# Kernel optimization log

Measured on AMD Instinct MI355X. Metric: run time of the kernel, lower is better.

Reference implementation:

```python
import jax, jax.numpy as jnp
import numpy as np

N_BINS = 20


def setup_inputs() -> dict:
    key = jax.random.key(0)
    k1, k2 = jax.random.split(key)
    softmaxes = jax.random.uniform(k1, (1000000, 100), dtype=jnp.float32)
    labels = jax.random.randint(k2, (1000000,), 0, 100, dtype=jnp.int64)
    return {"softmaxes": softmaxes, "labels": labels}


def reference(softmaxes, labels):
    num = softmaxes.shape[0]
    window = num // N_BINS  # equal-frequency bin size

    confidences = jnp.max(softmaxes, axis=1)
    predictions = jnp.argmax(softmaxes, axis=1)
    accuracies = (predictions == labels).astype(softmaxes.dtype)

    order = jnp.argsort(confidences)  # ascending, like torch.sort
    conf_sorted = confidences[order]
    acc_sorted = accuracies[order]

    # only full windows are flushed in the original loop
    n_used = N_BINS * window
    conf_bins = conf_sorted[:n_used].reshape(N_BINS, window)
    acc_bins = acc_sorted[:n_used].reshape(N_BINS, window)

    avg_conf = conf_bins.mean(axis=1)  # [N_BINS]
    avg_acc = acc_bins.mean(axis=1)    # [N_BINS] == ys list

    ece = jnp.sum(jnp.abs(avg_conf - avg_acc)) * (window / num)
    return ece.reshape(1), avg_acc
```

## Files before the change

### kernel.cpp

```cpp
#include <hip/hip_runtime.h>
#include <hip/hip_bf16.h>
#include <math.h>
#include <stdint.h>

#define NROWS 1000000
#define NCOLS 100
#define NBINS 20
#define NB    19
#define W     50000u
#define NH    2049

#define HIST_DW 0u
#define BINS_DW 2052u
#define ZERO_DW 2132u
#define CONF_DW 2136u

#define GLOAD_LDS16(g, l) __builtin_amdgcn_global_load_lds(                    \
    (const __attribute__((address_space(1))) void*)(g),                        \
    (__attribute__((address_space(3))) void*)(l), 16, 0, 0)

__device__ __forceinline__ unsigned int bucket_of(unsigned int bits) {
    if (bits < 0x3F000000u) return 0u;
    unsigned int t = (bits >> 12) - 258048u + 1u;
    return t > 2048u ? 2048u : t;
}

__global__ __launch_bounds__(256) void k1_rowmax(const float* __restrict__ x,
                                                 const int* __restrict__ labels,
                                                 float* __restrict__ conf,
                                                 unsigned int* __restrict__ zero_region) {
    __shared__ float4 ldsx4[1600];
    __shared__ unsigned long long ldsk[64];
    const float* ldsx = (const float*)ldsx4;
    int tid = threadIdx.x;
    int gtid = blockIdx.x * 256 + tid;
    if (gtid < (int)ZERO_DW) zero_region[gtid] = 0u;

    const int NTILES = NROWS / 64;
    const float4* xb = reinterpret_cast<const float4*>(x);
    for (int tile = blockIdx.x; tile < NTILES; tile += gridDim.x) {
        const float4* src = xb + (size_t)tile * 1600;
        int lab = 0;
        if (tid < 64) lab = labels[tile * 64 + tid];
        int wbase = tid & 192;
        #pragma unroll
        for (int i = 0; i < 6; i++) {
            int v = i * 256 + tid;
            GLOAD_LDS16(src + v, ldsx4 + i * 256 + wbase);
        }
        if (tid < 64) GLOAD_LDS16(src + 1536 + tid, ldsx4 + 1536);
        if (tid < 64) ldsk[tid] = 0ull;
        __syncthreads();
        int r = tid >> 2, q = tid & 3;
        const float* rowp = ldsx + r * 100 + q * 25;
        float best = rowp[0]; int bi = 0;
        #pragma unroll
        for (int k = 1; k < 25; k++) {
            float vv = rowp[k];
            if (vv > best) { best = vv; bi = k; }
        }
        unsigned long long key =
            ((unsigned long long)__float_as_uint(best) << 32)
            | (unsigned int)(NCOLS - (q * 25 + bi));
        atomicMax(&ldsk[r], key);
        __syncthreads();
        if (tid < 64) {
            unsigned long long kk = ldsk[tid];
            unsigned int bits = (unsigned int)(kk >> 32);
            int idx = NCOLS - (int)(kk & 0xFFFFFFFFu);
            if (idx == lab) bits |= 0x80000000u;
            conf[tile * 64 + tid] = __uint_as_float(bits);
        }
        __syncthreads();
    }
}

__global__ __launch_bounds__(512) void k2_hist(const float* __restrict__ conf,
                                               unsigned int* __restrict__ hist) {
    __shared__ unsigned int lh[NH];
    for (int i = threadIdx.x; i < NH; i += 512) lh[i] = 0u;
    __syncthreads();
    const uint4* c4 = reinterpret_cast<const uint4*>(conf);
    int stride = gridDim.x * 512;
    for (int i = blockIdx.x * 512 + threadIdx.x; i < NROWS / 4; i += stride) {
        uint4 v = c4[i];
        atomicAdd(&lh[bucket_of(v.x & 0x7FFFFFFFu)], 1u);
        atomicAdd(&lh[bucket_of(v.y & 0x7FFFFFFFu)], 1u);
        atomicAdd(&lh[bucket_of(v.z & 0x7FFFFFFFu)], 1u);
        atomicAdd(&lh[bucket_of(v.w & 0x7FFFFFFFu)], 1u);
    }
    __syncthreads();
    for (int i = threadIdx.x; i < NH; i += 512) {
        unsigned int c = lh[i];
        if (c) atomicAdd(&hist[i], c);
    }
}

__global__ __launch_bounds__(256) void k3_accum(const float* __restrict__ conf,
                                                const unsigned int* __restrict__ hist,
                                                double* __restrict__ bins) {
    __shared__ unsigned int ptab[NH];
    __shared__ unsigned int s[256];
    __shared__ unsigned int bndS[NB];
    __shared__ float sFr[NB];
    __shared__ float sc[4][NBINS], sa[4][NBINS];
    int tid = threadIdx.x;

    unsigned int loc[9];
    unsigned int tot = 0;
    int base = tid * 9;
    #pragma unroll
    for (int k = 0; k < 9; k++) {
        int idx = base + k;
        unsigned int v = (idx < NH) ? hist[idx] : 0u;
        loc[k] = tot; tot += v;
    }
    s[tid] = tot; __syncthreads();
    for (int off = 1; off < 256; off <<= 1) {
        unsigned int v = (tid >= off) ? s[tid - off] : 0u;
        __syncthreads();
        s[tid] += v;
        __syncthreads();
    }
    unsigned int excl = s[tid] - tot;
    #pragma unroll
    for (int k = 0; k < 9; k++) {
        int idx = base + k;
        if (idx < NH) ptab[idx] = excl + loc[k];
    }
    for (int i = tid; i < 4 * NBINS; i += 256) { (&sc[0][0])[i] = 0.f; (&sa[0][0])[i] = 0.f; }
    __syncthreads();

    if (tid < NB) {
        unsigned int r = (unsigned int)(tid + 1) * W;
        int lo = 0, hi = NH - 1;
        while (lo < hi) {
            int mid = (lo + hi + 1) >> 1;
            if (ptab[mid] <= r) lo = mid; else hi = mid - 1;
        }
        unsigned int p = ptab[lo];
        if (p < r) {
            unsigned int cnt = ((lo + 1 < NH) ? ptab[lo + 1] : (unsigned int)NROWS) - p;
            bndS[tid] = (unsigned int)lo;
            sFr[tid]  = (float)(r - p) / (float)cnt;
        } else {
            bndS[tid] = 0xFFFFFFFFu;
        }
    }
    __syncthreads();
    if (tid < NB && bndS[tid] != 0xFFFFFFFFu)
        ptab[bndS[tid]] |= (unsigned int)(tid + 1) << 24;
    __syncthreads();

    int wid = tid >> 6;
    const uint4* c4 = reinterpret_cast<const uint4*>(conf);
    int stride = gridDim.x * 256;
    for (int i = blockIdx.x * 256 + tid; i < NROWS / 4; i += stride) {
        uint4 q = c4[i];
        unsigned int bs[4] = { q.x, q.y, q.z, q.w };
        #pragma unroll
        for (int j = 0; j < 4; j++) {
            unsigned int raw = bs[j];
            float a = (float)(raw >> 31);
            unsigned int bits = raw & 0x7FFFFFFFu;
            float c = __uint_as_float(bits);
            unsigned int e = ptab[bucket_of(bits)];
            unsigned int t = e >> 24;
            if (t == 0u) {
                unsigned int bin = (e & 0xFFFFFFu) / W;
                atomicAdd(&sc[wid][bin], c); atomicAdd(&sa[wid][bin], a);
            } else {
                float fr = sFr[t - 1];
                atomicAdd(&sc[wid][t - 1], c * fr);
                atomicAdd(&sc[wid][t],     c * (1.f - fr));
                atomicAdd(&sa[wid][t - 1], a * fr);
                atomicAdd(&sa[wid][t],     a * (1.f - fr));
            }
        }
    }
    __syncthreads();
    if (tid < NBINS) {
        float tc = sc[0][tid] + sc[1][tid] + sc[2][tid] + sc[3][tid];
        float ta = sa[0][tid] + sa[1][tid] + sa[2][tid] + sa[3][tid];
        atomicAdd(&bins[tid],         (double)tc);
        atomicAdd(&bins[NBINS + tid], (double)ta);
    }
}

__global__ __launch_bounds__(64) void k4_final(const double* __restrict__ bins,
                                               float* __restrict__ out) {
    if (threadIdx.x == 0) {
        double ece = 0.0;
        for (int b = 0; b < NBINS; b++) {
            double avc = bins[b] / (double)W;
            double ava = bins[NBINS + b] / (double)W;
            ece += fabs(avc - ava);
            out[1 + b] = (float)ava;
        }
        out[0] = (float)(ece * ((double)W / (double)NROWS));
    }
}

extern "C" void kernel_launch(void* const* d_in, const int* in_sizes, int n_in,
                              void* d_out, int out_size, void* d_ws, size_t ws_size,
                              hipStream_t stream) {
    const float* x      = (const float*)d_in[0];
    const int*   labels = (const int*)d_in[1];
    float*       out    = (float*)d_out;
    unsigned int* wd    = (unsigned int*)d_ws;

    unsigned int* hist = wd + HIST_DW;
    double*       bins = (double*)(wd + BINS_DW);
    float*        conf = (float*)(wd + CONF_DW);

    k1_rowmax<<<2048, 256, 0, stream>>>(x, labels, conf, wd);
    k2_hist  <<<128, 512, 0, stream>>>(conf, hist);
    k3_accum <<<512, 256, 0, stream>>>(conf, hist, bins);
    k4_final <<<1, 64, 0, stream>>>(bins, out);
}
```

Before: 115.7 us.

## Double-buffer row tiles in rowmax kernel and use shuffle argmax reduction

The row-max kernel now double-buffers LDS tiles, issuing async global-to-LDS loads for the next tile before computing on the current one, with explicit vmcnt waits and raw barriers. The 64-bit LDS atomicMax reduction is replaced by intra-quad shuffle reductions that keep the lowest index on ties. Each thread that owns a row loads its label directly. The aim is to hide global load latency in this memory-bound pass and cut barriers and LDS atomics. The cost is double the LDS per block, which may lower occupancy, and fragile manual waitcnt handling.

```diff
diff --git a/kernel.cpp b/kernel.cpp
--- a/kernel.cpp
+++ b/kernel.cpp
@@ -29,50 +29,71 @@
                                                  const int* __restrict__ labels,
                                                  float* __restrict__ conf,
                                                  unsigned int* __restrict__ zero_region) {
-    __shared__ float4 ldsx4[1600];
-    __shared__ unsigned long long ldsk[64];
-    const float* ldsx = (const float*)ldsx4;
+    __shared__ float4 ldsx4[3200];
     int tid = threadIdx.x;
     int gtid = blockIdx.x * 256 + tid;
     if (gtid < (int)ZERO_DW) zero_region[gtid] = 0u;
 
     const int NTILES = NROWS / 64;
     const float4* xb = reinterpret_cast<const float4*>(x);
-    for (int tile = blockIdx.x; tile < NTILES; tile += gridDim.x) {
-        const float4* src = xb + (size_t)tile * 1600;
-        int lab = 0;
-        if (tid < 64) lab = labels[tile * 64 + tid];
-        int wbase = tid & 192;
-        #pragma unroll
-        for (int i = 0; i < 6; i++) {
-            int v = i * 256 + tid;
-            GLOAD_LDS16(src + v, ldsx4 + i * 256 + wbase);
-        }
-        if (tid < 64) GLOAD_LDS16(src + 1536 + tid, ldsx4 + 1536);
-        if (tid < 64) ldsk[tid] = 0ull;
-        __syncthreads();
-        int r = tid >> 2, q = tid & 3;
-        const float* rowp = ldsx + r * 100 + q * 25;
+    int lane = tid & 63;
+    int w    = tid >> 6;
+    int lab_next = 0, lab_cur = 0;
+
+    float4* bufA = ldsx4;
+    float4* bufB = ldsx4 + 1600;
+
+#define K1_ISSUE(t, buf)                                                       \
+    do {                                                                       \
+        const float4* src_ = xb + (size_t)(t) * 1600;                          \
+        _Pragma("unroll")                                                      \
+        for (int i_ = 0; i_ < 6; i_++)                                         \
+            GLOAD_LDS16(src_ + i_ * 256 + tid, (buf) + i_ * 256 + (tid & 192));\
+        if (lane < 16)                                                         \
+            GLOAD_LDS16(src_ + 1536 + 16 * w + lane, (buf) + 1536 + 16 * w);   \
+        if ((tid & 3) == 0) lab_next = labels[(t) * 64 + (tid >> 2)];          \
+    } while (0)
+
+    int tile = blockIdx.x;
+    if (tile < NTILES) K1_ISSUE(tile, bufA);
+
+    while (tile < NTILES) {
+        lab_cur = lab_next;
+        int nxt = tile + gridDim.x;
+        if (nxt < NTILES) {
+            K1_ISSUE(nxt, bufB);
+            asm volatile("s_waitcnt vmcnt(8)" ::: "memory");
+        } else {
+            asm volatile("s_waitcnt vmcnt(0)" ::: "memory");
+        }
+        __builtin_amdgcn_sched_barrier(0);
+        __builtin_amdgcn_s_barrier();
+
+        const float* rowp = (const float*)bufA + (tid >> 2) * 100 + (tid & 3) * 25;
         float best = rowp[0]; int bi = 0;
         #pragma unroll
         for (int k = 1; k < 25; k++) {
             float vv = rowp[k];
             if (vv > best) { best = vv; bi = k; }
         }
-        unsigned long long key =
-            ((unsigned long long)__float_as_uint(best) << 32)
-            | (unsigned int)(NCOLS - (q * 25 + bi));
-        atomicMax(&ldsk[r], key);
-        __syncthreads();
-        if (tid < 64) {
-            unsigned long long kk = ldsk[tid];
-            unsigned int bits = (unsigned int)(kk >> 32);
-            int idx = NCOLS - (int)(kk & 0xFFFFFFFFu);
-            if (idx == lab) bits |= 0x80000000u;
-            conf[tile * 64 + tid] = __uint_as_float(bits);
-        }
-        __syncthreads();
-    }
+        bi += (tid & 3) * 25;
+        #pragma unroll
+        for (int mask = 1; mask <= 2; mask <<= 1) {
+            float ov = __shfl_xor(best, mask);
+            int   oi = __shfl_xor(bi,   mask);
+            if (ov > best || (ov == best && oi < bi)) { best = ov; bi = oi; }
+        }
+        if ((tid & 3) == 0) {
+            unsigned int bits = __float_as_uint(best);
+            if (bi == lab_cur) bits |= 0x80000000u;
+            conf[tile * 64 + (tid >> 2)] = __uint_as_float(bits);
+        }
+        __builtin_amdgcn_s_barrier();
+
+        float4* tmp = bufA; bufA = bufB; bufB = tmp;
+        tile = nxt;
+    }
+#undef K1_ISSUE
 }
 
 __global__ __launch_bounds__(512) void k2_hist(const float* __restrict__ conf,
```

Measured after the change: 115.3 us, median of 2. About the same (-0.4%).
